# Performance work log

Measured on AMD Instinct MI355X. Metric: run time of the kernel, lower is better.

The kernel has to match this reference:

```python
import jax, jax.numpy as jnp
import numpy as np

NUM_FRAMES = 64
H, W = 2048, 2048
MAX_DEPTH = 12


def setup_inputs() -> dict:
    key = jax.random.key(0)
    k1, k2, k3 = jax.random.split(key, 3)
    frame_colors = jax.random.uniform(k1, (NUM_FRAMES, 3), dtype=jnp.float32)
    frame_selection = jax.random.uniform(k2, (NUM_FRAMES, 2, NUM_FRAMES), dtype=jnp.float32)
    split_ratios = jax.random.uniform(k3, (NUM_FRAMES,), dtype=jnp.float32)
    return {
        "frame_colors": frame_colors,
        "frame_selection": frame_selection,
        "split_ratios": split_ratios,
    }


def reference(frame_colors, frame_selection, split_ratios):
    """Vectorized per-pixel descent of the bounded fractal recursion.

    Instead of recursive slice-assignments with host-synced argmax/.item(),
    each pixel tracks (frame idx, region origin, region size) and descends
    MAX_DEPTH levels via gathers. Equivalent math to render_frame(0,...).
    """
    # Per-frame child indices (argmax over the selection logits).
    left_child = jnp.argmax(frame_selection[:, 0, :], axis=-1).astype(jnp.int32)   # [F]
    right_child = jnp.argmax(frame_selection[:, 1, :], axis=-1).astype(jnp.int32)  # [F]

    yy, xx = jnp.meshgrid(jnp.arange(H, dtype=jnp.int32),
                          jnp.arange(W, dtype=jnp.int32), indexing="ij")  # [H,W]

    idx = jnp.zeros((H, W), jnp.int32)   # current frame index per pixel
    y0 = jnp.zeros((H, W), jnp.int32)    # region origin
    x0 = jnp.zeros((H, W), jnp.int32)
    h = jnp.full((H, W), H, jnp.int32)   # region size
    w = jnp.full((H, W), W, jnp.int32)
    done = jnp.zeros((H, W), bool)

    for _ in range(MAX_DEPTH):
        leaf = (w < 2) | (h < 2)            # base case: region too small
        act = (~done) & (~leaf)             # pixels that descend this level
        done = done | leaf

        ratio = split_ratios[idx]                       # [H,W]
        is_vert = (idx % 2) == 1                        # split_directions = i % 2
        # left_width = max(1, int(width * ratio)); analogous top_height
        lw = jnp.maximum(1, jnp.floor(w.astype(jnp.float32) * ratio).astype(jnp.int32))
        th = jnp.maximum(1, jnp.floor(h.astype(jnp.float32) * ratio).astype(jnp.int32))

        go_left = jnp.where(is_vert, (xx - x0) < lw, (yy - y0) < th)
        child = jnp.where(go_left, left_child[idx], right_child[idx])

        nx0 = jnp.where(is_vert & (~go_left), x0 + lw, x0)
        nw = jnp.where(is_vert, jnp.where(go_left, lw, w - lw), w)
        ny0 = jnp.where((~is_vert) & (~go_left), y0 + th, y0)
        nh = jnp.where(~is_vert, jnp.where(go_left, th, h - th), h)

        idx = jnp.where(act, child, idx)
        x0 = jnp.where(act, nx0, x0)
        w = jnp.where(act, nw, w)
        y0 = jnp.where(act, ny0, y0)
        h = jnp.where(act, nh, h)

    # Fill each pixel with its leaf frame's background color -> [3, H, W]
    out = frame_colors[idx]                 # [H, W, 3]
    return jnp.transpose(out, (2, 0, 1))
```

## Files before the change

kernel.cpp:

```cpp
#include <hip/hip_runtime.h>

#define HH_DIM 2048
#define WW_DIM 2048
#define NF 64
#define MAX_DEPTH 12

__global__ void prep_kernel(const float* __restrict__ sel,
                            const float* __restrict__ ratios,
                            const float* __restrict__ colors,
                            float2* __restrict__ node,
                            float4* __restrict__ cpack) {
    __shared__ int s_child[2 * NF];
    int t = threadIdx.x;
    if (t < 2 * NF) {
        const float* row = sel + t * NF;
        float best = row[0];
        int bi = 0;
        #pragma unroll
        for (int j = 1; j < NF; ++j) {
            float v = row[j];
            if (v > best) { best = v; bi = j; }
        }
        s_child[t] = bi;
    }
    __syncthreads();
    if (t < NF) {
        int packed = s_child[2 * t] | (s_child[2 * t + 1] << 16);
        node[t] = make_float2(ratios[t], __int_as_float(packed));
        cpack[t] = make_float4(colors[3 * t], colors[3 * t + 1], colors[3 * t + 2], 0.0f);
    }
}

__global__ __launch_bounds__(256)
void render_kernel(const float2* __restrict__ node,
                   const float4* __restrict__ cpack,
                   float* __restrict__ out) {
    __shared__ float2 s_node[NF];
    __shared__ float4 s_col[NF];

    int t = threadIdx.x;
    if (t < NF)            s_node[t] = node[t];
    else if (t < 2 * NF)   s_col[t - NF] = cpack[t - NF];
    __syncthreads();

    int gid = blockIdx.x * 256 + t;
    int y  = gid >> 9;
    int xb = (gid & 511) << 2;

    int idx = 0, rx = xb, ry = y, w = WW_DIM, h = HH_DIM;
    int d = 0;
    bool div = false;
    for (; d < MAX_DEPTH; ++d) {
        if (w < 2 || h < 2) break;
        float2 nd = s_node[idx];
        int pk = __float_as_int(nd.y);
        int lc = pk & 0xffff, rcld = pk >> 16;
        bool vert = (idx & 1) != 0;
        int cs  = vert ? w  : h;
        int rc0 = vert ? rx : ry;
        int ls = (int)((float)cs * nd.x);
        ls = ls < 1 ? 1 : ls;
        if (vert & (rx < ls) & (ls <= rx + 3)) { div = true; break; }
        bool left = rc0 < ls;
        idx = left ? lc : rcld;
        int nr = left ? rc0 : rc0 - ls;
        int ns = left ? ls  : cs - ls;
        if (vert) { rx = nr; w = ns; } else { ry = nr; h = ns; }
    }

    int fidx0 = idx, fidx1 = idx, fidx2 = idx, fidx3 = idx;

    if (div) {
        int pidx[4], prx[4], pry[4], pw[4], ph[4];
        #pragma unroll
        for (int p = 0; p < 4; ++p) {
            pidx[p] = idx; prx[p] = rx + p; pry[p] = ry; pw[p] = w; ph[p] = h;
        }
        #pragma unroll 1
        for (int dd = d; dd < MAX_DEPTH; ++dd) {
            #pragma unroll
            for (int p = 0; p < 4; ++p) {
                float2 nd = s_node[pidx[p]];
                int pk = __float_as_int(nd.y);
                int lc = pk & 0xffff, rcld = pk >> 16;
                bool vert = (pidx[p] & 1) != 0;
                int cs  = vert ? pw[p]  : ph[p];
                int rc0 = vert ? prx[p] : pry[p];
                int ls = (int)((float)cs * nd.x);
                ls = ls < 1 ? 1 : ls;
                bool left = rc0 < ls;
                bool act = (pw[p] > 1) && (ph[p] > 1);
                int child = left ? lc : rcld;
                pidx[p] = act ? child : pidx[p];
                int nr = left ? rc0 : rc0 - ls;
                int ns = left ? ls  : cs - ls;
                if (vert) { prx[p] = nr; pw[p] = ns; }
                else      { pry[p] = nr; ph[p] = ns; }
            }
        }
        fidx0 = pidx[0]; fidx1 = pidx[1]; fidx2 = pidx[2]; fidx3 = pidx[3];
    }

    float4 k0 = s_col[fidx0];
    float4 k1 = s_col[fidx1];
    float4 k2 = s_col[fidx2];
    float4 k3 = s_col[fidx3];

    int base = y * WW_DIM + xb;
    const int plane = HH_DIM * WW_DIM;
    *(float4*)(out + base)             = make_float4(k0.x, k1.x, k2.x, k3.x);
    *(float4*)(out + plane + base)     = make_float4(k0.y, k1.y, k2.y, k3.y);
    *(float4*)(out + 2 * plane + base) = make_float4(k0.z, k1.z, k2.z, k3.z);
}

extern "C" void kernel_launch(void* const* d_in, const int* in_sizes, int n_in,
                              void* d_out, int out_size, void* d_ws, size_t ws_size,
                              hipStream_t stream) {
    const float* frame_colors    = (const float*)d_in[0];
    const float* frame_selection = (const float*)d_in[1];
    const float* split_ratios    = (const float*)d_in[2];
    float* out = (float*)d_out;

    float2* node  = (float2*)d_ws;
    float4* cpack = (float4*)((char*)d_ws + 1024);

    prep_kernel<<<1, 128, 0, stream>>>(frame_selection, split_ratios,
                                       frame_colors, node, cpack);
    render_kernel<<<4096, 256, 0, stream>>>(node, cpack, out);
}
```

Before: 99.85 us.

## Descend all four pixels independently with float arithmetic and full unrolling

```diff
diff --git a/kernel.cpp b/kernel.cpp
--- a/kernel.cpp
+++ b/kernel.cpp
@@ -47,64 +47,45 @@
     int y  = gid >> 9;
     int xb = (gid & 511) << 2;
 
-    int idx = 0, rx = xb, ry = y, w = WW_DIM, h = HH_DIM;
-    int d = 0;
-    bool div = false;
-    for (; d < MAX_DEPTH; ++d) {
-        if (w < 2 || h < 2) break;
-        float2 nd = s_node[idx];
-        int pk = __float_as_int(nd.y);
-        int lc = pk & 0xffff, rcld = pk >> 16;
-        bool vert = (idx & 1) != 0;
-        int cs  = vert ? w  : h;
-        int rc0 = vert ? rx : ry;
-        int ls = (int)((float)cs * nd.x);
-        ls = ls < 1 ? 1 : ls;
-        if (vert & (rx < ls) & (ls <= rx + 3)) { div = true; break; }
-        bool left = rc0 < ls;
-        idx = left ? lc : rcld;
-        int nr = left ? rc0 : rc0 - ls;
-        int ns = left ? ls  : cs - ls;
-        if (vert) { rx = nr; w = ns; } else { ry = nr; h = ns; }
+    int   idx[4];
+    float rx[4], ry[4], w[4], h[4];
+    #pragma unroll
+    for (int p = 0; p < 4; ++p) {
+        idx[p] = 0;
+        rx[p] = (float)(xb + p);
+        ry[p] = (float)y;
+        w[p]  = (float)WW_DIM;
+        h[p]  = (float)HH_DIM;
     }
 
-    int fidx0 = idx, fidx1 = idx, fidx2 = idx, fidx3 = idx;
-
-    if (div) {
-        int pidx[4], prx[4], pry[4], pw[4], ph[4];
+    #pragma unroll
+    for (int d = 0; d < MAX_DEPTH; ++d) {
         #pragma unroll
         for (int p = 0; p < 4; ++p) {
-            pidx[p] = idx; prx[p] = rx + p; pry[p] = ry; pw[p] = w; ph[p] = h;
+            float2 nd = s_node[idx[p]];
+            int   pk  = __float_as_int(nd.y);
+            bool  vert = (idx[p] & 1) != 0;
+            float cs = vert ? w[p]  : h[p];
+            float rc = vert ? rx[p] : ry[p];
+            float ls = floorf(cs * nd.x);
+            ls = fmaxf(ls, 1.0f);
+            bool left = rc < ls;
+            int  child = (pk >> (left ? 0 : 16)) & 63;
+            bool act = fminf(w[p], h[p]) >= 2.0f;
+            idx[p] = act ? child : idx[p];
+            float rc2 = left ? rc : rc - ls;
+            float ns  = left ? ls : cs - ls;
+            rx[p] = vert ? rc2  : rx[p];
+            ry[p] = vert ? ry[p] : rc2;
+            w[p]  = vert ? ns   : w[p];
+            h[p]  = vert ? h[p] : ns;
         }
-        #pragma unroll 1
-        for (int dd = d; dd < MAX_DEPTH; ++dd) {
-            #pragma unroll
-            for (int p = 0; p < 4; ++p) {
-                float2 nd = s_node[pidx[p]];
-                int pk = __float_as_int(nd.y);
-                int lc = pk & 0xffff, rcld = pk >> 16;
-                bool vert = (pidx[p] & 1) != 0;
-                int cs  = vert ? pw[p]  : ph[p];
-                int rc0 = vert ? prx[p] : pry[p];
-                int ls = (int)((float)cs * nd.x);
-                ls = ls < 1 ? 1 : ls;
-                bool left = rc0 < ls;
-                bool act = (pw[p] > 1) && (ph[p] > 1);
-                int child = left ? lc : rcld;
-                pidx[p] = act ? child : pidx[p];
-                int nr = left ? rc0 : rc0 - ls;
-                int ns = left ? ls  : cs - ls;
-                if (vert) { prx[p] = nr; pw[p] = ns; }
-                else      { pry[p] = nr; ph[p] = ns; }
-            }
-        }
-        fidx0 = pidx[0]; fidx1 = pidx[1]; fidx2 = pidx[2]; fidx3 = pidx[3];
     }
 
-    float4 k0 = s_col[fidx0];
-    float4 k1 = s_col[fidx1];
-    float4 k2 = s_col[fidx2];
-    float4 k3 = s_col[fidx3];
+    float4 k0 = s_col[idx[0]];
+    float4 k1 = s_col[idx[1]];
+    float4 k2 = s_col[idx[2]];
+    float4 k3 = s_col[idx[3]];
 
     int base = y * WW_DIM + xb;
     const int plane = HH_DIM * WW_DIM;
```

New measurement: 95.29 us. 1.05x faster.
